# Kernel optimization log

Measured on AMD Instinct MI355X. Metric: run time of the kernel, lower is better.

## Reference

```python
import jax, jax.numpy as jnp
import numpy as np

NUM_MID = 10   # hard-coded num_mid_nodes in HiPool.__init__
NUM_HIGH = 5   # ceil(10 / 2)


def map_low_to_high(num_low, num_high):
    # eye(num_high) repeat_interleaved by ceil(low/high) rows, truncated to num_low
    # == one-hot of i // edges_per_high
    edges_per_high = -(-num_low // num_high)
    return jax.nn.one_hot(jnp.arange(num_low) // edges_per_high, num_high,
                          dtype=jnp.float32)  # [low, high]


def cluster_attention(x, mapping, att):
    # x: [s, d], mapping: [s, m], att: [d, d]
    mid = mapping.T @ x                              # [m, d]
    scores = (mid @ att) @ x.T                       # [m, s]
    scores = scores * (1.0 - mapping).T              # zero (not -inf) own-cluster entries, as in source
    scores = jax.nn.softmax(scores, axis=1)
    return scores @ x + mid                          # [m, d]


def dense_gcn(x, adj, W, b):
    # torch_geometric DenseGCNConv with add_loop=True
    n = adj.shape[0]
    i = jnp.arange(n)
    adj = adj.at[i, i].set(1.0)
    deg = jnp.clip(jnp.sum(adj, axis=-1), 1.0, None) ** -0.5
    adj = deg[:, None] * adj * deg[None, :]
    return adj @ (x @ W) + b


def setup_inputs() -> dict:
    key = jax.random.key(0)
    ks = jax.random.split(key, 8)
    S, D, H = 8192, 768, 768
    return {
        "x": jax.random.normal(ks[0], (S, D), dtype=jnp.float32),
        "adjacency_matrix": jax.random.uniform(ks[1], (S, S), dtype=jnp.float32),
        "att_low_mid": jax.random.normal(ks[2], (D, D), dtype=jnp.float32) * 0.04,  # xavier_normal-ish
        "conv1_w": jax.random.normal(ks[3], (D, H), dtype=jnp.float32) * 0.04,
        "conv1_b": jnp.zeros((H,), dtype=jnp.float32),
        "att_mid_high": jax.random.normal(ks[4], (H, H), dtype=jnp.float32) * 0.04,
        "conv2_w": jax.random.normal(ks[5], (H, H), dtype=jnp.float32) * 0.04,
        "conv2_b": jnp.zeros((H,), dtype=jnp.float32),
    }


def reference(x, adjacency_matrix, att_low_mid, conv1_w, conv1_b,
              att_mid_high, conv2_w, conv2_b):
    s = x.shape[0]
    m1 = map_low_to_high(s, NUM_MID)                         # [s, 10]
    mid_adj = m1.T @ adjacency_matrix @ m1                   # [10, 10]
    mid_rep = cluster_attention(x, m1, att_low_mid)          # [10, d]
    x_mid = jax.nn.relu(dense_gcn(mid_rep, mid_adj, conv1_w, conv1_b))
    # F.dropout(...)[0]: dropout treated as identity (eval); [0] just dropped the batch dim
    m2 = map_low_to_high(NUM_MID, NUM_HIGH)                  # [10, 5]
    high_adj = m2.T @ mid_adj @ m2                           # [5, 5]
    high_rep = cluster_attention(x_mid, m2, att_mid_high)    # [5, h]
    out = jax.nn.relu(dense_gcn(high_rep, high_adj, conv2_w, conv2_b))
    return out.mean(axis=0)                                  # [h]
```

## Files before the change

### kernel.cpp

```cpp
#include <hip/hip_runtime.h>

constexpr int S    = 8192;
constexpr int D    = 768;
constexpr int NMID = 10;
constexpr int EPH  = 820;

constexpr int PART_ADJ = 0;
constexpr int PART_MID = 1024;
constexpr int OFF_ZB   = 123904;
constexpr int OFF_MATT = 123904;
constexpr int OFF_MREP = 131584;
constexpr int OFF_Y1   = 139264;
constexpr int OFF_Z2   = 146944;
constexpr int OFF_Y2   = 150784;
constexpr int ZERO_N   = 30720;
constexpr int OFF_MID  = 154624;
constexpr int OFF_XMID = 162304;
constexpr int OFF_SC   = 169984;
constexpr int OFF_SCB  = 251904;

template <int NR>
__device__ __forceinline__ void mm_core(const float* __restrict__ W,
                                        const float* mi,
                                        float* __restrict__ out, int kb) {
    int c = threadIdx.x;
    float a0[NR], a1[NR], a2[NR];
#pragma unroll
    for (int i = 0; i < NR; ++i) { a0[i] = 0.f; a1[i] = 0.f; a2[i] = 0.f; }
    for (int kk = 0; kk < 16; ++kk) {
        const float* wr = W + (size_t)(kb + kk) * D;
        float w0 = wr[c], w1 = wr[c + 256], w2 = wr[c + 512];
#pragma unroll
        for (int i = 0; i < NR; ++i) {
            float m = mi[i * 16 + kk];
            a0[i] += m * w0; a1[i] += m * w1; a2[i] += m * w2;
        }
    }
#pragma unroll
    for (int i = 0; i < NR; ++i) {
        atomicAdd(&out[i * D + c],       a0[i]);
        atomicAdd(&out[i * D + c + 256], a1[i]);
        atomicAdd(&out[i * D + c + 512], a2[i]);
    }
}

__global__ __launch_bounds__(256) void k_big(const float* __restrict__ A,
                                             const float* __restrict__ x,
                                             float* __restrict__ ws) {
    int bx = blockIdx.x;
    int tid = threadIdx.x;
    if (bx < 800) {
        __shared__ float red[256];
        int p = bx >> 3, sp = bx & 7;
        int i = p / 10, j = p % 10;
        int r0 = i * EPH, r1 = min(r0 + EPH, S);
        int c0 = j * EPH, c1 = min(c0 + EPH, S);
        int nr = r1 - r0;
        int rs0 = r0 + (nr * sp) / 8, rs1 = r0 + (nr * (sp + 1)) / 8;
        int nc4 = (c1 - c0) >> 2;
        float acc = 0.f;
        for (int r = rs0; r < rs1; ++r) {
            const float4* row = (const float4*)(A + (size_t)r * S + c0);
            for (int t = tid; t < nc4; t += 256) {
                float4 v = row[t];
                acc += (v.x + v.y) + (v.z + v.w);
            }
        }
        red[tid] = acc;
        __syncthreads();
        for (int off = 128; off > 0; off >>= 1) {
            if (tid < off) red[tid] += red[tid + off];
            __syncthreads();
        }
        if (tid == 0) ws[PART_ADJ + bx] = red[0];
    } else if (bx < 1280) {
        int b  = bx - 800;
        int cl = b / 48;
        int rem = b % 48;
        int cc = rem / 16, sp = rem % 16;
        int r0 = cl * EPH, r1 = min(r0 + EPH, S);
        int nr = r1 - r0;
        int rs0 = r0 + (nr * sp) / 16, rs1 = r0 + (nr * (sp + 1)) / 16;
        int c = cc * 256 + tid;
        float acc = 0.f;
        for (int r = rs0; r < rs1; ++r) acc += x[(size_t)r * D + c];
        ws[PART_MID + (sp * NMID + cl) * D + c] = acc;
    } else {
        int b = bx - 1280;
        for (int t = b * 256 + tid; t < ZERO_N; t += 16 * 256)
            ws[OFF_ZB + t] = 0.f;
    }
}

__global__ __launch_bounds__(256) void k_mmA(const float* __restrict__ attL,
                                             float* __restrict__ ws) {
    __shared__ float mi[160];
    int kb = blockIdx.x * 16;
    int tid = threadIdx.x;
    if (tid < 160) {
        int cl = tid >> 4, k = tid & 15;
        float s = 0.f;
#pragma unroll
        for (int sp = 0; sp < 16; ++sp)
            s += ws[PART_MID + (sp * NMID + cl) * D + kb + k];
        mi[tid] = s;
        ws[OFF_MID + cl * D + kb + k] = s;
    }
    __syncthreads();
    mm_core<10>(attL, mi, ws + OFF_MATT, kb);
}

__global__ __launch_bounds__(256) void k_scores(const float* __restrict__ x,
                                                float* __restrict__ ws) {
    __shared__ float ma[NMID * D];
    __shared__ float scl[32 * NMID];
    int tid = threadIdx.x;
    for (int t = tid; t < NMID * D; t += 256) ma[t] = ws[OFF_MATT + t];
    __syncthreads();
    const float4* maf = (const float4*)ma;
    const float4* x4  = (const float4*)x;
    int wave = tid >> 6, ln = tid & 63;
    int rbase = blockIdx.x * 32 + wave * 8;
    for (int rr = 0; rr < 8; ++rr) {
        int r = rbase + rr;
        float4 v0 = x4[(size_t)r * 192 + ln];
        float4 v1 = x4[(size_t)r * 192 + 64 + ln];
        float4 v2 = x4[(size_t)r * 192 + 128 + ln];
        int rc = r / EPH;
#pragma unroll
        for (int i = 0; i < NMID; ++i) {
            float4 m0 = maf[i * 192 + ln];
            float4 m1 = maf[i * 192 + 64 + ln];
            float4 m2 = maf[i * 192 + 128 + ln];
            float p = m0.x * v0.x + m0.y * v0.y + m0.z * v0.z + m0.w * v0.w
                    + m1.x * v1.x + m1.y * v1.y + m1.z * v1.z + m1.w * v1.w
                    + m2.x * v2.x + m2.y * v2.y + m2.z * v2.z + m2.w * v2.w;
#pragma unroll
            for (int off = 32; off > 0; off >>= 1) p += __shfl_down(p, off, 64);
            if (ln == 0) {
                float v = (rc == i) ? 0.f : p;
                ws[OFF_SC + r * NMID + i] = v;
                scl[(wave * 8 + rr) * NMID + i] = v;
            }
        }
    }
    __syncthreads();
    if (tid < NMID) {
        float m = -1e30f;
        for (int r = 0; r < 32; ++r) m = fmaxf(m, scl[r * NMID + tid]);
        float s = 0.f;
        for (int r = 0; r < 32; ++r) s += expf(scl[r * NMID + tid] - m);
        ws[OFF_SCB + blockIdx.x * 20 + tid * 2]     = m;
        ws[OFF_SCB + blockIdx.x * 20 + tid * 2 + 1] = s;
    }
}

__global__ __launch_bounds__(192) void k_pv(const float* __restrict__ x,
                                            float* __restrict__ ws) {
    __shared__ float lm[160], ls[160], Mi[10], Inv[10], p[64 * NMID];
    int tid = threadIdx.x;
    if (tid < 160) {
        int i = tid >> 4, seg = tid & 15;
        float m = -1e30f;
        for (int b = seg * 16; b < seg * 16 + 16; ++b)
            m = fmaxf(m, ws[OFF_SCB + b * 20 + i * 2]);
        float s = 0.f;
        for (int b = seg * 16; b < seg * 16 + 16; ++b)
            s += ws[OFF_SCB + b * 20 + i * 2 + 1] *
                 expf(ws[OFF_SCB + b * 20 + i * 2] - m);
        lm[tid] = m; ls[tid] = s;
    }
    __syncthreads();
    if (tid < NMID) {
        float M = -1e30f;
        for (int g = 0; g < 16; ++g) M = fmaxf(M, lm[tid * 16 + g]);
        float Ssum = 0.f;
        for (int g = 0; g < 16; ++g) Ssum += ls[tid * 16 + g] * expf(lm[tid * 16 + g] - M);
        Mi[tid] = M; Inv[tid] = 1.f / Ssum;
    }
    __syncthreads();
    int r0 = blockIdx.x * 64;
    for (int t = tid; t < 64 * NMID; t += 192) {
        int i = t % NMID;
        p[t] = expf(ws[OFF_SC + r0 * NMID + t] - Mi[i]) * Inv[i];
    }
    __syncthreads();
    const float4* x4 = (const float4*)x;
    float4 acc[NMID];
#pragma unroll
    for (int i = 0; i < NMID; ++i) acc[i] = make_float4(0.f, 0.f, 0.f, 0.f);
    for (int r = 0; r < 64; ++r) {
        float4 xv = x4[(size_t)(r0 + r) * 192 + tid];
#pragma unroll
        for (int i = 0; i < NMID; ++i) {
            float pv = p[r * NMID + i];
            acc[i].x += pv * xv.x; acc[i].y += pv * xv.y;
            acc[i].z += pv * xv.z; acc[i].w += pv * xv.w;
        }
    }
#pragma unroll
    for (int i = 0; i < NMID; ++i) {
        float* base = ws + OFF_MREP + i * D + tid * 4;
        atomicAdd(base + 0, acc[i].x);
        atomicAdd(base + 1, acc[i].y);
        atomicAdd(base + 2, acc[i].z);
        atomicAdd(base + 3, acc[i].w);
    }
}

__global__ __launch_bounds__(256) void k_mmB(const float* __restrict__ W1,
                                             float* __restrict__ ws) {
    __shared__ float mi[160];
    int kb = blockIdx.x * 16;
    int tid = threadIdx.x;
    if (tid < 160) {
        int cl = tid >> 4, k = tid & 15;
        mi[tid] = ws[OFF_MID + cl * D + kb + k] + ws[OFF_MREP + cl * D + kb + k];
    }
    __syncthreads();
    mm_core<10>(W1, mi, ws + OFF_Y1, kb);
}

__global__ __launch_bounds__(256) void k_mmC(const float* __restrict__ attH,
                                             const float* __restrict__ b1,
                                             float* __restrict__ ws) {
    __shared__ float aa[100], dg[10], NM[100], xml[160], mi[80];
    int tid = threadIdx.x;
    if (tid < 100) {
        float s = 0.f;
#pragma unroll
        for (int sp = 0; sp < 8; ++sp) s += ws[PART_ADJ + tid * 8 + sp];
        aa[tid] = s;
    }
    __syncthreads();
    if (tid < 10) {
        float s = 0.f;
#pragma unroll
        for (int j = 0; j < 10; ++j) s += (tid == j) ? 1.0f : aa[tid * 10 + j];
        dg[tid] = 1.0f / sqrtf(fmaxf(s, 1.0f));
    }
    __syncthreads();
    if (tid < 100) {
        int i = tid / 10, j = tid % 10;
        NM[tid] = dg[i] * ((i == j) ? 1.0f : aa[tid]) * dg[j];
    }
    __syncthreads();
    int kb = blockIdx.x * 16;
    if (tid < 160) {
        int i = tid >> 4, c = kb + (tid & 15);
        float s = b1[c];
#pragma unroll
        for (int j = 0; j < 10; ++j) s += NM[i * 10 + j] * ws[OFF_Y1 + j * D + c];
        float xm = fmaxf(s, 0.f);
        ws[OFF_XMID + i * D + c] = xm;
        xml[tid] = xm;
    }
    __syncthreads();
    if (tid < 80) {
        int a = tid >> 4, k = tid & 15;
        mi[tid] = xml[(2 * a) * 16 + k] + xml[(2 * a + 1) * 16 + k];
    }
    __syncthreads();
    mm_core<5>(attH, mi, ws + OFF_Z2, kb);
}

__global__ __launch_bounds__(256) void k_mmD(const float* __restrict__ W2,
                                             float* __restrict__ ws) {
    __shared__ float s2[64], P2[50], mi[80];
    int tid = threadIdx.x, wv = tid >> 6, ln = tid & 63;
    for (int pp = wv; pp < 50; pp += 4) {
        int i = pp / 10, r = pp % 10;
        const float4* za = (const float4*)(ws + OFF_Z2 + i * D);
        const float4* xa = (const float4*)(ws + OFF_XMID + r * D);
        float acc = 0.f;
#pragma unroll
        for (int q = 0; q < 3; ++q) {
            float4 a = za[q * 64 + ln], b = xa[q * 64 + ln];
            acc += a.x * b.x + a.y * b.y + a.z * b.z + a.w * b.w;
        }
#pragma unroll
        for (int off = 32; off > 0; off >>= 1) acc += __shfl_down(acc, off, 64);
        if (ln == 0) s2[pp] = ((r >> 1) == i) ? 0.f : acc;
    }
    __syncthreads();
    if (tid < 5) {
        float mx = -1e30f;
#pragma unroll
        for (int r = 0; r < 10; ++r) mx = fmaxf(mx, s2[tid * 10 + r]);
        float sm = 0.f; float e[10];
#pragma unroll
        for (int r = 0; r < 10; ++r) { e[r] = expf(s2[tid * 10 + r] - mx); sm += e[r]; }
#pragma unroll
        for (int r = 0; r < 10; ++r) P2[tid * 10 + r] = e[r] / sm;
    }
    __syncthreads();
    int kb = blockIdx.x * 16;
    if (tid < 80) {
        int i = tid >> 4, c = kb + (tid & 15);
        float xm[10];
#pragma unroll
        for (int r = 0; r < 10; ++r) xm[r] = ws[OFF_XMID + r * D + c];
        float o = xm[2 * i] + xm[2 * i + 1];
#pragma unroll
        for (int r = 0; r < 10; ++r) o += P2[i * 10 + r] * xm[r];
        mi[tid] = o;
    }
    __syncthreads();
    mm_core<5>(W2, mi, ws + OFF_Y2, kb);
}

__global__ __launch_bounds__(768) void k_final(const float* __restrict__ b2,
                                               const float* __restrict__ ws,
                                               float* __restrict__ out) {
    __shared__ float aa[100], ha[25], dh[5], NH[25];
    int tid = threadIdx.x;
    if (tid < 100) {
        float s = 0.f;
#pragma unroll
        for (int sp = 0; sp < 8; ++sp) s += ws[PART_ADJ + tid * 8 + sp];
        aa[tid] = s;
    }
    __syncthreads();
    if (tid < 25) {
        int a = tid / 5, b = tid % 5;
        ha[tid] = aa[(2 * a) * 10 + 2 * b] + aa[(2 * a) * 10 + 2 * b + 1]
                + aa[(2 * a + 1) * 10 + 2 * b] + aa[(2 * a + 1) * 10 + 2 * b + 1];
    }
    __syncthreads();
    if (tid < 5) {
        float s = 0.f;
#pragma unroll
        for (int j = 0; j < 5; ++j) s += (tid == j) ? 1.0f : ha[tid * 5 + j];
        dh[tid] = 1.0f / sqrtf(fmaxf(s, 1.0f));
    }
    __syncthreads();
    if (tid < 25) {
        int i = tid / 5, j = tid % 5;
        NH[tid] = dh[i] * ((i == j) ? 1.0f : ha[tid]) * dh[j];
    }
    __syncthreads();
    int c = tid;
    float y[5];
#pragma unroll
    for (int j = 0; j < 5; ++j) y[j] = ws[OFF_Y2 + j * D + c];
    float bias = b2[c];
    float s = 0.f;
#pragma unroll
    for (int i = 0; i < 5; ++i) {
        float v = bias;
#pragma unroll
        for (int j = 0; j < 5; ++j) v += NH[i * 5 + j] * y[j];
        s += fmaxf(v, 0.f);
    }
    out[c] = s * 0.2f;
}

extern "C" void kernel_launch(void* const* d_in, const int* in_sizes, int n_in,
                              void* d_out, int out_size, void* d_ws, size_t ws_size,
                              hipStream_t stream) {
    const float* x    = (const float*)d_in[0];
    const float* adj  = (const float*)d_in[1];
    const float* attL = (const float*)d_in[2];
    const float* W1   = (const float*)d_in[3];
    const float* b1   = (const float*)d_in[4];
    const float* attH = (const float*)d_in[5];
    const float* W2   = (const float*)d_in[6];
    const float* b2   = (const float*)d_in[7];
    float* ws  = (float*)d_ws;
    float* out = (float*)d_out;

    k_big   <<<1296, 256, 0, stream>>>(adj, x, ws);
    k_mmA   <<<48,   256, 0, stream>>>(attL, ws);
    k_scores<<<256,  256, 0, stream>>>(x, ws);
    k_pv    <<<128,  192, 0, stream>>>(x, ws);
    k_mmB   <<<48,   256, 0, stream>>>(W1, ws);
    k_mmC   <<<48,   256, 0, stream>>>(attH, b1, ws);
    k_mmD   <<<48,   256, 0, stream>>>(W2, ws);
    k_final <<<1,    768, 0, stream>>>(b2, ws, out);
}
```

Baseline: 165.9 us.

## Spread adjacency reduction across dependent kernels to overlap with small GEMM stages

The 256MB adjacency block-sum is split into 3200 work items and distributed as extra blocks across the first five kernels. It now runs alongside the low-occupancy mid-attention and matmul stages instead of entirely in the first kernel. The PV stage also switches from atomicAdd to per-block partial outputs that k5 reduces, and uses 128-row tiles with 256 threads. This adds a 64-way partial reduction and more workspace traffic in exchange for hiding the latency of the small serial kernels.

```diff
diff --git a/kernel.cpp b/kernel.cpp
--- a/kernel.cpp
+++ b/kernel.cpp
@@ -6,18 +6,56 @@
 constexpr int EPH  = 820;
 
 constexpr int PART_ADJ = 0;
-constexpr int PART_MID = 1024;
-constexpr int OFF_ZB   = 123904;
-constexpr int OFF_MATT = 123904;
-constexpr int OFF_MREP = 131584;
-constexpr int OFF_Y1   = 139264;
-constexpr int OFF_Z2   = 146944;
-constexpr int OFF_Y2   = 150784;
-constexpr int ZERO_N   = 30720;
-constexpr int OFF_MID  = 154624;
-constexpr int OFF_XMID = 162304;
-constexpr int OFF_SC   = 169984;
-constexpr int OFF_SCB  = 251904;
+constexpr int PART_MID = 3200;
+constexpr int OFF_ZB   = 64640;
+constexpr int OFF_MATT = 64640;
+constexpr int OFF_Y1   = 72320;
+constexpr int OFF_Z2   = 80000;
+constexpr int OFF_Y2   = 83840;
+constexpr int ZERO_N   = 23040;
+constexpr int OFF_MID  = 87680;
+constexpr int OFF_XMID = 95360;
+constexpr int OFF_SC   = 103040;
+constexpr int OFF_SCB  = 184960;
+constexpr int OFF_PVP  = 190080;
+
+__device__ __forceinline__ void adj_partial(const float* __restrict__ A,
+                                            float* __restrict__ ws, int item) {
+    __shared__ float wred[4];
+    int p = item >> 5, s = item & 31;
+    int i = p / 10, j = p % 10;
+    int r0 = i * EPH, nr = min(EPH, S - r0);
+    int c0 = j * EPH, nc = min(EPH, S - c0);
+    int rs0 = r0 + (nr * s) / 32, rs1 = r0 + (nr * (s + 1)) / 32;
+    int nc4 = nc >> 2;
+    int tid = threadIdx.x;
+    float acc = 0.f;
+    for (int r = rs0; r < rs1; ++r) {
+        const float4* row = (const float4*)(A + (size_t)r * S + c0);
+        if (tid < nc4) {
+            float4 v = row[tid];
+            acc += (v.x + v.y) + (v.z + v.w);
+        }
+    }
+#pragma unroll
+    for (int off = 32; off > 0; off >>= 1) acc += __shfl_down(acc, off, 64);
+    int ln = tid & 63, wv = tid >> 6;
+    if (ln == 0) wred[wv] = acc;
+    __syncthreads();
+    if (tid == 0) ws[PART_ADJ + item] = (wred[0] + wred[1]) + (wred[2] + wred[3]);
+}
+
+__device__ __forceinline__ void mid_partial(const float* __restrict__ x,
+                                            float* __restrict__ ws, int item) {
+    int cl = item / 24, rem = item % 24;
+    int cc = rem >> 3, sp = rem & 7;
+    int r0 = cl * EPH, nr = min(EPH, S - r0);
+    int rs0 = r0 + (nr * sp) / 8, rs1 = r0 + (nr * (sp + 1)) / 8;
+    int c = cc * 256 + threadIdx.x;
+    float acc = 0.f;
+    for (int r = rs0; r < rs1; ++r) acc += x[(size_t)r * D + c];
+    ws[PART_MID + (sp * NMID + cl) * D + c] = acc;
+}
 
 template <int NR>
 __device__ __forceinline__ void mm_core(const float* __restrict__ W,
@@ -44,64 +82,31 @@
     }
 }
 
-__global__ __launch_bounds__(256) void k_big(const float* __restrict__ A,
-                                             const float* __restrict__ x,
-                                             float* __restrict__ ws) {
-    int bx = blockIdx.x;
-    int tid = threadIdx.x;
-    if (bx < 800) {
-        __shared__ float red[256];
-        int p = bx >> 3, sp = bx & 7;
-        int i = p / 10, j = p % 10;
-        int r0 = i * EPH, r1 = min(r0 + EPH, S);
-        int c0 = j * EPH, c1 = min(c0 + EPH, S);
-        int nr = r1 - r0;
-        int rs0 = r0 + (nr * sp) / 8, rs1 = r0 + (nr * (sp + 1)) / 8;
-        int nc4 = (c1 - c0) >> 2;
-        float acc = 0.f;
-        for (int r = rs0; r < rs1; ++r) {
-            const float4* row = (const float4*)(A + (size_t)r * S + c0);
-            for (int t = tid; t < nc4; t += 256) {
-                float4 v = row[t];
-                acc += (v.x + v.y) + (v.z + v.w);
-            }
-        }
-        red[tid] = acc;
-        __syncthreads();
-        for (int off = 128; off > 0; off >>= 1) {
-            if (tid < off) red[tid] += red[tid + off];
-            __syncthreads();
-        }
-        if (tid == 0) ws[PART_ADJ + bx] = red[0];
-    } else if (bx < 1280) {
-        int b  = bx - 800;
-        int cl = b / 48;
-        int rem = b % 48;
-        int cc = rem / 16, sp = rem % 16;
-        int r0 = cl * EPH, r1 = min(r0 + EPH, S);
-        int nr = r1 - r0;
-        int rs0 = r0 + (nr * sp) / 16, rs1 = r0 + (nr * (sp + 1)) / 16;
-        int c = cc * 256 + tid;
-        float acc = 0.f;
-        for (int r = rs0; r < rs1; ++r) acc += x[(size_t)r * D + c];
-        ws[PART_MID + (sp * NMID + cl) * D + c] = acc;
-    } else {
-        int b = bx - 1280;
-        for (int t = b * 256 + tid; t < ZERO_N; t += 16 * 256)
+__global__ __launch_bounds__(256) void k1(const float* __restrict__ A,
+                                          const float* __restrict__ x,
+                                          float* __restrict__ ws) {
+    int bx = blockIdx.x;
+    if (bx < 800) adj_partial(A, ws, bx);
+    else if (bx < 1040) mid_partial(x, ws, bx - 800);
+    else {
+        int b = bx - 1040;
+        for (int t = b * 256 + threadIdx.x; t < ZERO_N; t += 16 * 256)
             ws[OFF_ZB + t] = 0.f;
     }
 }
 
-__global__ __launch_bounds__(256) void k_mmA(const float* __restrict__ attL,
-                                             float* __restrict__ ws) {
+__global__ __launch_bounds__(256) void k2(const float* __restrict__ attL,
+                                          const float* __restrict__ A,
+                                          float* __restrict__ ws) {
+    int bx = blockIdx.x;
+    if (bx >= 48) { adj_partial(A, ws, 800 + bx - 48); return; }
     __shared__ float mi[160];
-    int kb = blockIdx.x * 16;
-    int tid = threadIdx.x;
+    int kb = bx * 16, tid = threadIdx.x;
     if (tid < 160) {
         int cl = tid >> 4, k = tid & 15;
         float s = 0.f;
 #pragma unroll
-        for (int sp = 0; sp < 16; ++sp)
+        for (int sp = 0; sp < 8; ++sp)
             s += ws[PART_MID + (sp * NMID + cl) * D + kb + k];
         mi[tid] = s;
         ws[OFF_MID + cl * D + kb + k] = s;
@@ -110,8 +115,11 @@
     mm_core<10>(attL, mi, ws + OFF_MATT, kb);
 }
 
-__global__ __launch_bounds__(256) void k_scores(const float* __restrict__ x,
-                                                float* __restrict__ ws) {
+__global__ __launch_bounds__(256) void k3(const float* __restrict__ x,
+                                          const float* __restrict__ A,
+                                          float* __restrict__ ws) {
+    int bx = blockIdx.x;
+    if (bx >= 256) { adj_partial(A, ws, 1600 + bx - 256); return; }
     __shared__ float ma[NMID * D];
     __shared__ float scl[32 * NMID];
     int tid = threadIdx.x;
@@ -120,7 +128,7 @@
     const float4* maf = (const float4*)ma;
     const float4* x4  = (const float4*)x;
     int wave = tid >> 6, ln = tid & 63;
-    int rbase = blockIdx.x * 32 + wave * 8;
+    int rbase = bx * 32 + wave * 8;
     for (int rr = 0; rr < 8; ++rr) {
         int r = rbase + rr;
         float4 v0 = x4[(size_t)r * 192 + ln];
@@ -150,14 +158,17 @@
         for (int r = 0; r < 32; ++r) m = fmaxf(m, scl[r * NMID + tid]);
         float s = 0.f;
         for (int r = 0; r < 32; ++r) s += expf(scl[r * NMID + tid] - m);
-        ws[OFF_SCB + blockIdx.x * 20 + tid * 2]     = m;
-        ws[OFF_SCB + blockIdx.x * 20 + tid * 2 + 1] = s;
-    }
-}
-
-__global__ __launch_bounds__(192) void k_pv(const float* __restrict__ x,
-                                            float* __restrict__ ws) {
-    __shared__ float lm[160], ls[160], Mi[10], Inv[10], p[64 * NMID];
+        ws[OFF_SCB + bx * 20 + tid * 2]     = m;
+        ws[OFF_SCB + bx * 20 + tid * 2 + 1] = s;
+    }
+}
+
+__global__ __launch_bounds__(256) void k4(const float* __restrict__ x,
+                                          const float* __restrict__ A,
+                                          float* __restrict__ ws) {
+    int bx = blockIdx.x;
+    if (bx >= 64) { adj_partial(A, ws, 2200 + bx - 64); return; }
+    __shared__ float lm[160], ls[160], Mi[10], Inv[10], p[128 * NMID];
     int tid = threadIdx.x;
     if (tid < 160) {
         int i = tid >> 4, seg = tid & 15;
@@ -179,57 +190,60 @@
         Mi[tid] = M; Inv[tid] = 1.f / Ssum;
     }
     __syncthreads();
-    int r0 = blockIdx.x * 64;
-    for (int t = tid; t < 64 * NMID; t += 192) {
+    int r0 = bx * 128;
+    for (int t = tid; t < 128 * NMID; t += 256) {
         int i = t % NMID;
         p[t] = expf(ws[OFF_SC + r0 * NMID + t] - Mi[i]) * Inv[i];
     }
     __syncthreads();
-    const float4* x4 = (const float4*)x;
-    float4 acc[NMID];
-#pragma unroll
-    for (int i = 0; i < NMID; ++i) acc[i] = make_float4(0.f, 0.f, 0.f, 0.f);
-    for (int r = 0; r < 64; ++r) {
-        float4 xv = x4[(size_t)(r0 + r) * 192 + tid];
+    float a0[NMID], a1[NMID], a2[NMID];
+#pragma unroll
+    for (int i = 0; i < NMID; ++i) { a0[i] = 0.f; a1[i] = 0.f; a2[i] = 0.f; }
+    for (int r = 0; r < 128; ++r) {
+        const float* xr = x + (size_t)(r0 + r) * D;
+        float x0 = xr[tid], x1 = xr[tid + 256], x2 = xr[tid + 512];
 #pragma unroll
         for (int i = 0; i < NMID; ++i) {
             float pv = p[r * NMID + i];
-            acc[i].x += pv * xv.x; acc[i].y += pv * xv.y;
-            acc[i].z += pv * xv.z; acc[i].w += pv * xv.w;
+            a0[i] += pv * x0; a1[i] += pv * x1; a2[i] += pv * x2;
         }
     }
 #pragma unroll
     for (int i = 0; i < NMID; ++i) {
-        float* base = ws + OFF_MREP + i * D + tid * 4;
-        atomicAdd(base + 0, acc[i].x);
-        atomicAdd(base + 1, acc[i].y);
-        atomicAdd(base + 2, acc[i].z);
-        atomicAdd(base + 3, acc[i].w);
-    }
-}
-
-__global__ __launch_bounds__(256) void k_mmB(const float* __restrict__ W1,
-                                             float* __restrict__ ws) {
+        float* base = ws + OFF_PVP + (bx * NMID + i) * D;
+        base[tid]       = a0[i];
+        base[tid + 256] = a1[i];
+        base[tid + 512] = a2[i];
+    }
+}
+
+__global__ __launch_bounds__(256) void k5(const float* __restrict__ W1,
+                                          const float* __restrict__ A,
+                                          float* __restrict__ ws) {
+    int bx = blockIdx.x;
+    if (bx >= 48) { adj_partial(A, ws, 2800 + bx - 48); return; }
     __shared__ float mi[160];
-    int kb = blockIdx.x * 16;
-    int tid = threadIdx.x;
+    int kb = bx * 16, tid = threadIdx.x;
     if (tid < 160) {
         int cl = tid >> 4, k = tid & 15;
-        mi[tid] = ws[OFF_MID + cl * D + kb + k] + ws[OFF_MREP + cl * D + kb + k];
+        float s = ws[OFF_MID + cl * D + kb + k];
+        for (int b = 0; b < 64; ++b)
+            s += ws[OFF_PVP + (b * NMID + cl) * D + kb + k];
+        mi[tid] = s;
     }
     __syncthreads();
     mm_core<10>(W1, mi, ws + OFF_Y1, kb);
 }
 
-__global__ __launch_bounds__(256) void k_mmC(const float* __restrict__ attH,
-                                             const float* __restrict__ b1,
-                                             float* __restrict__ ws) {
+__global__ __launch_bounds__(256) void k6(const float* __restrict__ attH,
+                                          const float* __restrict__ b1,
+                                          float* __restrict__ ws) {
     __shared__ float aa[100], dg[10], NM[100], xml[160], mi[80];
     int tid = threadIdx.x;
     if (tid < 100) {
         float s = 0.f;
 #pragma unroll
-        for (int sp = 0; sp < 8; ++sp) s += ws[PART_ADJ + tid * 8 + sp];
+        for (int sp = 0; sp < 32; ++sp) s += ws[PART_ADJ + tid * 32 + sp];
         aa[tid] = s;
     }
     __syncthreads();
@@ -264,8 +278,8 @@
     mm_core<5>(attH, mi, ws + OFF_Z2, kb);
 }
 
-__global__ __launch_bounds__(256) void k_mmD(const float* __restrict__ W2,
-                                             float* __restrict__ ws) {
+__global__ __launch_bounds__(256) void k7(const float* __restrict__ W2,
+                                          float* __restrict__ ws) {
     __shared__ float s2[64], P2[50], mi[80];
     int tid = threadIdx.x, wv = tid >> 6, ln = tid & 63;
     for (int pp = wv; pp < 50; pp += 4) {
@@ -309,15 +323,15 @@
     mm_core<5>(W2, mi, ws + OFF_Y2, kb);
 }
 
-__global__ __launch_bounds__(768) void k_final(const float* __restrict__ b2,
-                                               const float* __restrict__ ws,
-                                               float* __restrict__ out) {
+__global__ __launch_bounds__(768) void k8(const float* __restrict__ b2,
+                                          const float* __restrict__ ws,
+                                          float* __restrict__ out) {
     __shared__ float aa[100], ha[25], dh[5], NH[25];
     int tid = threadIdx.x;
     if (tid < 100) {
         float s = 0.f;
 #pragma unroll
-        for (int sp = 0; sp < 8; ++sp) s += ws[PART_ADJ + tid * 8 + sp];
+        for (int sp = 0; sp < 32; ++sp) s += ws[PART_ADJ + tid * 32 + sp];
         aa[tid] = s;
     }
     __syncthreads();
@@ -369,12 +383,12 @@
     float* ws  = (float*)d_ws;
     float* out = (float*)d_out;
 
-    k_big   <<<1296, 256, 0, stream>>>(adj, x, ws);
-    k_mmA   <<<48,   256, 0, stream>>>(attL, ws);
-    k_scores<<<256,  256, 0, stream>>>(x, ws);
-    k_pv    <<<128,  192, 0, stream>>>(x, ws);
-    k_mmB   <<<48,   256, 0, stream>>>(W1, ws);
-    k_mmC   <<<48,   256, 0, stream>>>(attH, b1, ws);
-    k_mmD   <<<48,   256, 0, stream>>>(W2, ws);
-    k_final <<<1,    768, 0, stream>>>(b2, ws, out);
-}
+    k1<<<1056, 256, 0, stream>>>(adj, x, ws);
+    k2<<<848,  256, 0, stream>>>(attL, adj, ws);
+    k3<<<856,  256, 0, stream>>>(x, adj, ws);
+    k4<<<664,  256, 0, stream>>>(x, adj, ws);
+    k5<<<448,  256, 0, stream>>>(W1, adj, ws);
+    k6<<<48,   256, 0, stream>>>(attH, b1, ws);
+    k7<<<48,   256, 0, stream>>>(W2, ws);
+    k8<<<1,    768, 0, stream>>>(b2, ws, out);
+}
```

Measured after the change: 160.1 us. 3.5% less time.
